# Kernel tuning notes

Hardware: AMD Instinct MI355X
Metric: run time of the kernel (lower is better)

Reference implementation:

```python
import jax, jax.numpy as jnp
import numpy as np
from jax import lax

SMOOTH = 0.04


def setup_inputs() -> dict:
    key = jax.random.key(0)
    k1, k2 = jax.random.split(key)
    B, C, F, T = 8, 2, 257, 6000
    mag_spec = jax.random.uniform(k1, (B, C, F, T), dtype=jnp.float32)
    initial_state = jax.random.uniform(k2, (B, C, F, 1), dtype=jnp.float32)
    weights = jnp.full((1,), SMOOTH, dtype=jnp.float32)  # per_channel=False -> shape (1,)
    return {"mag_spec": mag_spec, "initial_state": initial_state, "weights": weights}


def reference(mag_spec, initial_state, weights):
    # EMA recurrence along the last (time) axis:
    #   acc_t = w * x_t + (1 - w) * acc_{t-1}
    w = jnp.clip(weights, 0.0, 1.0)  # (1,), broadcasts over [B,C,F]
    xs = jnp.moveaxis(mag_spec, -1, 0)  # [T, B, C, F]
    init = initial_state[..., 0]  # [B, C, F]

    def step(acc, x):
        acc = w * x + (1.0 - w) * acc
        return acc, acc

    _, ys = lax.scan(step, init, xs)  # ys: [T, B, C, F]
    return jnp.moveaxis(ys, 0, -1)  # [B, C, F, T]
```

## Files before the change

### kernel.cpp

```cpp
#include <hip/hip_runtime.h>


constexpr int T_LEN = 6000;
constexpr int OUT_C = 1500;
constexpr int NW    = 4;
constexpr int K     = 28;
constexpr int KF    = K / 4;
constexpr int E     = 64 * K;
constexpr int H     = E - OUT_C;
constexpr int HF    = H / 4;

static_assert(OUT_C % 4 == 0 && H % 4 == 0, "float4 alignment");
static_assert(NW * OUT_C == T_LEN, "chunks cover sequence");

__global__ __launch_bounds__(64 * NW) void ema_kernel(
    const float* __restrict__ x,
    const float* __restrict__ init,
    const float* __restrict__ wptr,
    float* __restrict__ out)
{
    const int seq  = blockIdx.x;
    const int wv   = threadIdx.x >> 6;
    const int lane = threadIdx.x & 63;

    const float w  = fminf(fmaxf(wptr[0], 0.0f), 1.0f);
    const float d  = 1.0f - w;
    const float iv = init[seq];

    const float4* g4 = (const float4*)(x + (size_t)seq * T_LEN);
    float4*       o4 = (float4*)(out + (size_t)seq * T_LEN);

    const int fbase = wv * (OUT_C / 4) - HF + lane * KF;

    float4 xv[KF];
    #pragma unroll
    for (int k = 0; k < KF; ++k) {
        int f = fbase + k;
        xv[k] = (f >= 0) ? g4[f] : make_float4(iv, iv, iv, iv);
    }

    float b = 0.0f;
    #pragma unroll
    for (int k = 0; k < KF; ++k) {
        b = fmaf(w, xv[k].x, d * b); xv[k].x = b;
        b = fmaf(w, xv[k].y, d * b); xv[k].y = b;
        b = fmaf(w, xv[k].z, d * b); xv[k].z = b;
        b = fmaf(w, xv[k].w, d * b); xv[k].w = b;
    }

    const float d2 = d * d, d4 = d2 * d2, d8 = d4 * d4, d16 = d8 * d8;
    float a = d16 * d8 * d4;

    #pragma unroll
    for (int off = 1; off < 64; off <<= 1) {
        float pa = __shfl_up(a, off, 64);
        float pb = __shfl_up(b, off, 64);
        if (lane >= off) {
            b = fmaf(a, pb, b);
            a = a * pa;
        }
    }
    float ea = __shfl_up(a, 1, 64);
    float eb = __shfl_up(b, 1, 64);
    if (lane == 0) { ea = 1.0f; eb = 0.0f; }

    const float s_in = fmaf(ea, iv, eb);

    float f1 = d * s_in;
    #pragma unroll
    for (int k = 0; k < KF; ++k) {
        xv[k].x += f1; f1 *= d;
        xv[k].y += f1; f1 *= d;
        xv[k].z += f1; f1 *= d;
        xv[k].w += f1; f1 *= d;
    }

    #pragma unroll
    for (int k = 0; k < KF; ++k) {
        int rel = lane * KF + k;
        if (rel >= HF) o4[fbase + k] = xv[k];
    }
}

extern "C" void kernel_launch(void* const* d_in, const int* in_sizes, int n_in,
                              void* d_out, int out_size, void* d_ws, size_t ws_size,
                              hipStream_t stream) {
    const float* mag_spec = (const float*)d_in[0];
    const float* initial_state = (const float*)d_in[1];
    const float* weights = (const float*)d_in[2];
    float* out = (float*)d_out;

    const int nseq = in_sizes[1];
    ema_kernel<<<nseq, 64 * NW, 0, stream>>>(mag_spec, initial_state, weights, out);
}
```

Before: 190.9 us.

## Stage EMA windows through LDS with coalesced loads and persistent prefetching waves

Each wave now loads its overlapping time window with coalesced float4 accesses (lane-strided) into shared memory instead of each lane reading a contiguous strided chunk. Lanes then run the scan from LDS. A persistent grid-stride loop over windows prefetches the next window into registers while the current one is processed. Output uses nontemporal stores. The per-lane chunk grows from 28 to 29 elements. The cost is extra LDS traffic and possible bank conflicts from the stride-29 per-lane access, plus more registers held by the double buffering.

New measurement: 250.0 us. 31.0% more time.

```diff
diff --git a/kernel.cpp b/kernel.cpp
--- a/kernel.cpp
+++ b/kernel.cpp
@@ -1,84 +1,124 @@
 #include <hip/hip_runtime.h>
 
 
-constexpr int T_LEN = 6000;
-constexpr int OUT_C = 1500;
-constexpr int NW    = 4;
-constexpr int K     = 28;
-constexpr int KF    = K / 4;
-constexpr int E     = 64 * K;
-constexpr int H     = E - OUT_C;
-constexpr int HF    = H / 4;
+constexpr int T_LEN  = 6000;
+constexpr int OUT_F4 = 375;
+constexpr int K      = 29;
+constexpr int E      = 64 * K;
+constexpr int EF4    = E / 4;
+constexpr int H      = E - 1500;
+constexpr int HF4    = H / 4;
+constexpr int WPS    = 4;
+constexpr int BLOCK  = 256;
+constexpr int NBLK   = 1024;
 
-static_assert(OUT_C % 4 == 0 && H % 4 == 0, "float4 alignment");
-static_assert(NW * OUT_C == T_LEN, "chunks cover sequence");
+typedef float vfloat4 __attribute__((ext_vector_type(4)));
 
-__global__ __launch_bounds__(64 * NW) void ema_kernel(
+__device__ __forceinline__ void load_window(float4 v[8], const float4* __restrict__ g4,
+                                            int win, int lane) {
+    const int base = win * OUT_F4 - HF4;
+    #pragma unroll
+    for (int r = 0; r < 8; ++r) {
+        const int f = r * 64 + lane;
+        if (f < EF4) {
+            int idx = base + f;
+            v[r] = g4[idx < 0 ? 0 : idx];
+        }
+    }
+}
+
+__global__ __launch_bounds__(BLOCK) void ema_kernel(
     const float* __restrict__ x,
     const float* __restrict__ init,
     const float* __restrict__ wptr,
-    float* __restrict__ out)
+    float* __restrict__ out,
+    int nwin)
 {
-    const int seq  = blockIdx.x;
+    __shared__ __align__(16) float tile[4][E];
     const int wv   = threadIdx.x >> 6;
     const int lane = threadIdx.x & 63;
+    float* T = tile[wv];
 
-    const float w  = fminf(fmaxf(wptr[0], 0.0f), 1.0f);
-    const float d  = 1.0f - w;
-    const float iv = init[seq];
+    const int gwave  = blockIdx.x * 4 + wv;
+    const int stride = gridDim.x * 4;
 
-    const float4* g4 = (const float4*)(x + (size_t)seq * T_LEN);
-    float4*       o4 = (float4*)(out + (size_t)seq * T_LEN);
+    const float w = fminf(fmaxf(wptr[0], 0.0f), 1.0f);
+    const float d = 1.0f - w;
+    const float d2 = d * d, d4 = d2 * d2, d8 = d4 * d4, d16 = d8 * d8;
+    const float d29 = d16 * d8 * d4 * d;
 
-    const int fbase = wv * (OUT_C / 4) - HF + lane * KF;
+    const float4* g4 = (const float4*)x;
+    float4*       o4 = (float4*)out;
 
-    float4 xv[KF];
-    #pragma unroll
-    for (int k = 0; k < KF; ++k) {
-        int f = fbase + k;
-        xv[k] = (f >= 0) ? g4[f] : make_float4(iv, iv, iv, iv);
-    }
+    float4 cur[8];
+    int win = gwave;
+    if (win < nwin) load_window(cur, g4, win, lane);
 
-    float b = 0.0f;
-    #pragma unroll
-    for (int k = 0; k < KF; ++k) {
-        b = fmaf(w, xv[k].x, d * b); xv[k].x = b;
-        b = fmaf(w, xv[k].y, d * b); xv[k].y = b;
-        b = fmaf(w, xv[k].z, d * b); xv[k].z = b;
-        b = fmaf(w, xv[k].w, d * b); xv[k].w = b;
-    }
+    for (; win < nwin; win += stride) {
+        #pragma unroll
+        for (int r = 0; r < 8; ++r) {
+            const int f = r * 64 + lane;
+            if (f < EF4) *(float4*)&T[f * 4] = cur[r];
+        }
 
-    const float d2 = d * d, d4 = d2 * d2, d8 = d4 * d4, d16 = d8 * d8;
-    float a = d16 * d8 * d4;
+        const float iv = init[win >> 2];
+        if ((win & (WPS - 1)) == 0) {
+            const float4 ivv = make_float4(iv, iv, iv, iv);
+            #pragma unroll
+            for (int r = 0; r < 2; ++r) {
+                const int f = r * 64 + lane;
+                if (f < HF4) *(float4*)&T[f * 4] = ivv;
+            }
+        }
 
-    #pragma unroll
-    for (int off = 1; off < 64; off <<= 1) {
-        float pa = __shfl_up(a, off, 64);
-        float pb = __shfl_up(b, off, 64);
-        if (lane >= off) {
-            b = fmaf(a, pb, b);
-            a = a * pa;
+        const int nxtwin = win + stride;
+        float4 nxt[8];
+        if (nxtwin < nwin) load_window(nxt, g4, nxtwin, lane);
+
+        asm volatile("s_waitcnt lgkmcnt(0)" ::: "memory");
+
+        const float* lx = &T[lane * K];
+        float b = 0.0f;
+        #pragma unroll
+        for (int j = 0; j < K; ++j) b = fmaf(w, lx[j], d * b);
+        float a = d29;
+
+        #pragma unroll
+        for (int off = 1; off < 64; off <<= 1) {
+            float pa = __shfl_up(a, off, 64);
+            float pb = __shfl_up(b, off, 64);
+            if (lane >= off) {
+                b = fmaf(a, pb, b);
+                a = a * pa;
+            }
         }
-    }
-    float ea = __shfl_up(a, 1, 64);
-    float eb = __shfl_up(b, 1, 64);
-    if (lane == 0) { ea = 1.0f; eb = 0.0f; }
+        float ea = __shfl_up(a, 1, 64);
+        float eb = __shfl_up(b, 1, 64);
+        if (lane == 0) { ea = 1.0f; eb = 0.0f; }
+        const float s_in = fmaf(ea, iv, eb);
 
-    const float s_in = fmaf(ea, iv, eb);
+        float* lxm = &T[lane * K];
+        float acc = s_in;
+        #pragma unroll
+        for (int j = 0; j < K; ++j) {
+            acc = fmaf(w, lxm[j], d * acc);
+            lxm[j] = acc;
+        }
 
-    float f1 = d * s_in;
-    #pragma unroll
-    for (int k = 0; k < KF; ++k) {
-        xv[k].x += f1; f1 *= d;
-        xv[k].y += f1; f1 *= d;
-        xv[k].z += f1; f1 *= d;
-        xv[k].w += f1; f1 *= d;
-    }
+        asm volatile("s_waitcnt lgkmcnt(0)" ::: "memory");
 
-    #pragma unroll
-    for (int k = 0; k < KF; ++k) {
-        int rel = lane * KF + k;
-        if (rel >= HF) o4[fbase + k] = xv[k];
+        vfloat4* ow = (vfloat4*)(o4 + (size_t)win * OUT_F4);
+        #pragma unroll
+        for (int s = 0; s < 6; ++s) {
+            const int f = s * 64 + lane;
+            if (f < OUT_F4) {
+                vfloat4 v = *(const vfloat4*)&T[H + f * 4];
+                __builtin_nontemporal_store(v, &ow[f]);
+            }
+        }
+
+        #pragma unroll
+        for (int r = 0; r < 8; ++r) cur[r] = nxt[r];
     }
 }
 
@@ -91,5 +131,7 @@
     float* out = (float*)d_out;
 
     const int nseq = in_sizes[1];
-    ema_kernel<<<nseq, 64 * NW, 0, stream>>>(mag_spec, initial_state, weights, out);
+    const int nwin = nseq * WPS;
+
+    ema_kernel<<<NBLK, BLOCK, 0, stream>>>(mag_spec, initial_state, weights, out, nwin);
 }
```
